# Performance work log

Hardware: AMD Instinct MI355X
Metric: run time of the kernel (lower is better)

Reference implementation:

```python
import jax, jax.numpy as jnp
import numpy as np

B, N = 8, 4096  # batch of epidemic trajectories, nodes in the contact network


def setup_inputs() -> dict:
    key = jax.random.key(0)
    k1, k2, k3, k4 = jax.random.split(key, 4)
    state = jax.random.uniform(k1, (B, 4, N), dtype=jnp.float32)
    state = state / state.sum(axis=1, keepdims=True)  # per-node SEIR distribution
    ISNet = jax.random.uniform(k2, (N, N), dtype=jnp.float32)  # dense contact weights in [0,1)
    # small transition probs so rows sum < 1 (expand_psMatrix stays a valid stochastic matrix)
    psMatrix = jax.random.uniform(k3, (4, 4), dtype=jnp.float32) * 0.05
    U = jax.random.uniform(k4, (N,), dtype=jnp.float32)  # torch.rand(n) draw, shared across batch
    return {"state": state, "ISNet": ISNet, "psMatrix": psMatrix, "U": U}


def _expand_ps(psMatrix):
    # eye * (1 - row_sum) + psMatrix  (adds the stay-in-state probability)
    stable = 1.0 - psMatrix.sum(axis=1)
    return jnp.eye(4, dtype=psMatrix.dtype) * stable + psMatrix


def _step(state, ISNet, psMatrix):
    psM = _expand_ps(psMatrix)
    p01 = psM[0, 1]
    # lp[b,j,k] = log(1 - ISNet[j,k] * S_b[j] * I_b[k] * p01)   (vectorized over batch)
    lp = jnp.log(1.0 - ISNet[None, :, :] * state[:, 0, :, None] * state[:, 2, None, :] * p01)
    ps1 = 1.0 - jnp.exp(lp.sum(axis=2))  # [B, N] infection probability per node
    zeros = jnp.zeros_like(ps1)
    ps10 = jnp.stack([1.0 - ps1, ps1, zeros, zeros], axis=1)  # [B, 4, N]
    # constantM zeroes the S row of psM before the transpose-matmul
    mask = jnp.array([[0.0, 0, 0, 0], [1, 1, 1, 1], [1, 1, 1, 1], [1, 1, 1, 1]], dtype=psM.dtype)
    ps2T = (psM * mask).T  # [4, 4]
    return state[:, 0][:, None, :] * ps10 + jnp.einsum('ij,bjn->bin', ps2T, state)


def _sample(P, U):
    # cumulative-threshold sampling: first compartment whose running sum crosses U fires
    u = jnp.broadcast_to(U[None, :], P[:, 0, :].shape)  # [B, N], shared draw across batch
    outs = []
    for i in range(P.shape[1]):  # fixed 4 compartments
        u = u - P[:, i, :]
        s = (u < 0).astype(P.dtype)
        outs.append(s)
        u = u + s
    return jnp.stack(outs, axis=1)  # [B, 4, N] one-hot per node


def reference(state, ISNet, psMatrix, U):
    new_state = _step(state, ISNet, psMatrix)
    return _sample(new_state, U)
```

## Files before the change

kernel.cpp:

```cpp
#include <hip/hip_runtime.h>

#define NN 4096
#define BB 8
#define JT 4


__device__ __forceinline__ float2 pk_mul(float2 a, float2 b) {
    return make_float2(a.x * b.x, a.y * b.y);
}
__device__ __forceinline__ float2 pk_add(float2 a, float2 b) {
    return make_float2(a.x + b.x, a.y + b.y);
}
__device__ __forceinline__ float2 pk_fnma(float2 a, float2 b, float2 c) {
    return make_float2(fmaf(-a.x, b.x, c.x), fmaf(-a.y, b.y, c.y));
}

__global__ __launch_bounds__(256) void epi_kernel(
    const float* __restrict__ state,
    const float* __restrict__ ISNet,
    const float* __restrict__ psMatrix,
    const float* __restrict__ U,
    float* __restrict__ out)
{
    const int j0   = blockIdx.x * JT;
    const int tid  = threadIdx.x;
    const int wave = tid >> 6;
    const int lane = tid & 63;
    const int b0   = wave * 2;

    const float p01 = psMatrix[1];

    float  cf[JT][2];
    double prod[JT][2];
    #pragma unroll
    for (int jj = 0; jj < JT; ++jj) {
        #pragma unroll
        for (int bi = 0; bi < 2; ++bi) {
            cf[jj][bi]   = state[(size_t)(b0 + bi) * 4 * NN + (j0 + jj)] * p01;
            prod[jj][bi] = 1.0;
        }
    }

    const float4* __restrict__ w0 = (const float4*)(ISNet + (size_t)(j0 + 0) * NN);
    const float4* __restrict__ w1 = (const float4*)(ISNet + (size_t)(j0 + 1) * NN);
    const float4* __restrict__ w2 = (const float4*)(ISNet + (size_t)(j0 + 2) * NN);
    const float4* __restrict__ w3 = (const float4*)(ISNet + (size_t)(j0 + 3) * NN);
    const float4* __restrict__ i0 = (const float4*)(state + ((size_t)(b0 + 0) * 4 + 2) * NN);
    const float4* __restrict__ i1 = (const float4*)(state + ((size_t)(b0 + 1) * 4 + 2) * NN);

    float4 wA[JT], wB[JT], iA[2], iB[2];

#define LOADSET(W, I, X)                                   \
    do {                                                   \
        const int _x = (X);                                \
        W[0] = w0[_x]; W[1] = w1[_x];                      \
        W[2] = w2[_x]; W[3] = w3[_x];                      \
        I[0] = i0[_x]; I[1] = i1[_x];                      \
    } while (0)

    auto compute = [&](const float4 (&W)[JT], const float4 (&I)[2]) {
        #pragma unroll
        for (int jj = 0; jj < JT; ++jj) {
            const float2 w01 = make_float2(W[jj].x, W[jj].y);
            const float2 w23 = make_float2(W[jj].z, W[jj].w);
            #pragma unroll
            for (int bi = 0; bi < 2; ++bi) {
                const float2 c2  = make_float2(cf[jj][bi], cf[jj][bi]);
                const float2 i01 = make_float2(I[bi].x, I[bi].y);
                const float2 i23 = make_float2(I[bi].z, I[bi].w);
                const float2 z01 = pk_mul(pk_mul(c2, w01), i01);
                const float2 z23 = pk_mul(pk_mul(c2, w23), i23);
                const float2 q2 = pk_fnma(z01, z23, pk_add(z01, z23));
                const float q = fmaf(-q2.x, q2.y, q2.x + q2.y);
                prod[jj][bi] = fma(-(double)q, prod[jj][bi], prod[jj][bi]);
            }
        }
    };

    LOADSET(wA, iA, lane);
    LOADSET(wB, iB, lane + 64);
    #pragma unroll
    for (int it = 0; it < 16; it += 2) {
        compute(wA, iA);
        if (it + 2 < 16) LOADSET(wA, iA, lane + (it + 2) * 64);
        compute(wB, iB);
        if (it + 3 < 16) LOADSET(wB, iB, lane + (it + 3) * 64);
    }
#undef LOADSET

    #pragma unroll
    for (int off = 32; off > 0; off >>= 1) {
        #pragma unroll
        for (int jj = 0; jj < JT; ++jj) {
            #pragma unroll
            for (int bi = 0; bi < 2; ++bi)
                prod[jj][bi] *= __shfl_down(prod[jj][bi], off, 64);
        }
    }

    __shared__ double red[JT][BB];
    if (lane == 0) {
        #pragma unroll
        for (int jj = 0; jj < JT; ++jj) {
            #pragma unroll
            for (int bi = 0; bi < 2; ++bi)
                red[jj][b0 + bi] = prod[jj][bi];
        }
    }
    __syncthreads();

    if (tid < JT * BB) {
        const int jj = tid >> 3, b = tid & 7;
        const int j  = j0 + jj;
        const double tot = red[jj][b];
        const double ps1 = 1.0 - tot;

        double pm[4][4];
        #pragma unroll
        for (int r = 0; r < 4; ++r) {
            double s = 0.0;
            #pragma unroll
            for (int q = 0; q < 4; ++q) {
                pm[r][q] = (double)psMatrix[r * 4 + q];
                s += pm[r][q];
            }
            pm[r][r] += (1.0 - s);
        }

        double st[4];
        #pragma unroll
        for (int r = 0; r < 4; ++r)
            st[r] = (double)state[(size_t)b * 4 * NN + r * NN + j];

        const double S = st[0];
        const double ps10[4] = {1.0 - ps1, ps1, 0.0, 0.0};

        double P[4];
        #pragma unroll
        for (int i = 0; i < 4; ++i) {
            double acc = S * ps10[i];
            #pragma unroll
            for (int r = 1; r < 4; ++r)
                acc += pm[r][i] * st[r];
            P[i] = acc;
        }

        double u = (double)U[j];
        #pragma unroll
        for (int i = 0; i < 4; ++i) {
            u -= P[i];
            const double s = (u < 0.0) ? 1.0 : 0.0;
            out[(size_t)b * 4 * NN + i * NN + j] = (float)s;
            u += s;
        }
    }
}

extern "C" void kernel_launch(void* const* d_in, const int* in_sizes, int n_in,
                              void* d_out, int out_size, void* d_ws, size_t ws_size,
                              hipStream_t stream) {
    const float* state    = (const float*)d_in[0];
    const float* ISNet    = (const float*)d_in[1];
    const float* psMatrix = (const float*)d_in[2];
    const float* U        = (const float*)d_in[3];
    float* out            = (float*)d_out;

    epi_kernel<<<NN / JT, 256, 0, stream>>>(state, ISNet, psMatrix, U, out);
}
```

Baseline: 24.18 us.

## Triple-buffer weight loads, split I loads, and use transpose-style wave reduction

Replaces the double-buffered combined loads with three rotating ISNet weight buffers prefetched three steps ahead and two I buffers prefetched two steps ahead. The goal is to hide more global memory latency. The per-wave reduction is reworked: xor shuffles reduce down to 8-lane groups, then each group selects one of the eight (j,b) products and finishes with three shuffles, which cuts total shuffle count. Launch bounds now request 4 blocks per CU, which may limit registers and cause spills given the extra buffers.

Measured after the change: 23.98 us. About the same (-0.9%).

```diff
diff --git a/kernel.cpp b/kernel.cpp
--- a/kernel.cpp
+++ b/kernel.cpp
@@ -15,7 +15,7 @@
     return make_float2(fmaf(-a.x, b.x, c.x), fmaf(-a.y, b.y, c.y));
 }
 
-__global__ __launch_bounds__(256) void epi_kernel(
+__global__ __launch_bounds__(256, 4) void epi_kernel(
     const float* __restrict__ state,
     const float* __restrict__ ISNet,
     const float* __restrict__ psMatrix,
@@ -48,14 +48,18 @@
     const float4* __restrict__ i0 = (const float4*)(state + ((size_t)(b0 + 0) * 4 + 2) * NN);
     const float4* __restrict__ i1 = (const float4*)(state + ((size_t)(b0 + 1) * 4 + 2) * NN);
 
-    float4 wA[JT], wB[JT], iA[2], iB[2];
+    float4 wA[JT], wB[JT], wC[JT], ia[2], ib[2];
 
-#define LOADSET(W, I, X)                                   \
-    do {                                                   \
-        const int _x = (X);                                \
-        W[0] = w0[_x]; W[1] = w1[_x];                      \
-        W[2] = w2[_x]; W[3] = w3[_x];                      \
-        I[0] = i0[_x]; I[1] = i1[_x];                      \
+#define LW(BUF, IDX)                                        \
+    do {                                                    \
+        const int _x = lane + (IDX) * 64;                   \
+        BUF[0] = w0[_x]; BUF[1] = w1[_x];                   \
+        BUF[2] = w2[_x]; BUF[3] = w3[_x];                   \
+    } while (0)
+#define LI(BUF, IDX)                                        \
+    do {                                                    \
+        const int _x = lane + (IDX) * 64;                   \
+        BUF[0] = i0[_x]; BUF[1] = i1[_x];                   \
     } while (0)
 
     auto compute = [&](const float4 (&W)[JT], const float4 (&I)[2]) {
@@ -70,43 +74,56 @@
                 const float2 i23 = make_float2(I[bi].z, I[bi].w);
                 const float2 z01 = pk_mul(pk_mul(c2, w01), i01);
                 const float2 z23 = pk_mul(pk_mul(c2, w23), i23);
-                const float2 q2 = pk_fnma(z01, z23, pk_add(z01, z23));
-                const float q = fmaf(-q2.x, q2.y, q2.x + q2.y);
+                const float2 q2  = pk_fnma(z01, z23, pk_add(z01, z23));
+                const float  q   = fmaf(-q2.x, q2.y, q2.x + q2.y);
                 prod[jj][bi] = fma(-(double)q, prod[jj][bi], prod[jj][bi]);
             }
         }
     };
 
-    LOADSET(wA, iA, lane);
-    LOADSET(wB, iB, lane + 64);
-    #pragma unroll
-    for (int it = 0; it < 16; it += 2) {
-        compute(wA, iA);
-        if (it + 2 < 16) LOADSET(wA, iA, lane + (it + 2) * 64);
-        compute(wB, iB);
-        if (it + 3 < 16) LOADSET(wB, iB, lane + (it + 3) * 64);
-    }
-#undef LOADSET
+#define STEP(W, I, K)                                       \
+    do {                                                    \
+        compute(W, I);                                      \
+        if ((K) + 3 < 16) LW(W, (K) + 3);                   \
+        if ((K) + 2 < 16) LI(I, (K) + 2);                   \
+    } while (0)
+
+    LW(wA, 0); LI(ia, 0); LW(wB, 1); LI(ib, 1); LW(wC, 2);
+
+    STEP(wA, ia, 0);  STEP(wB, ib, 1);  STEP(wC, ia, 2);  STEP(wA, ib, 3);
+    STEP(wB, ia, 4);  STEP(wC, ib, 5);  STEP(wA, ia, 6);  STEP(wB, ib, 7);
+    STEP(wC, ia, 8);  STEP(wA, ib, 9);  STEP(wB, ia, 10); STEP(wC, ib, 11);
+    STEP(wA, ia, 12); STEP(wB, ib, 13); STEP(wC, ia, 14); STEP(wA, ib, 15);
+#undef STEP
+#undef LW
+#undef LI
 
     #pragma unroll
-    for (int off = 32; off > 0; off >>= 1) {
+    for (int off = 32; off >= 8; off >>= 1) {
         #pragma unroll
         for (int jj = 0; jj < JT; ++jj) {
             #pragma unroll
             for (int bi = 0; bi < 2; ++bi)
-                prod[jj][bi] *= __shfl_down(prod[jj][bi], off, 64);
+                prod[jj][bi] *= __shfl_xor(prod[jj][bi], off, 64);
         }
     }
 
+    const int g = lane >> 3;
+    double v = prod[0][0];
+    v = (g == 1) ? prod[0][1] : v;
+    v = (g == 2) ? prod[1][0] : v;
+    v = (g == 3) ? prod[1][1] : v;
+    v = (g == 4) ? prod[2][0] : v;
+    v = (g == 5) ? prod[2][1] : v;
+    v = (g == 6) ? prod[3][0] : v;
+    v = (g == 7) ? prod[3][1] : v;
+    v *= __shfl_down(v, 4, 64);
+    v *= __shfl_down(v, 2, 64);
+    v *= __shfl_down(v, 1, 64);
+
     __shared__ double red[JT][BB];
-    if (lane == 0) {
-        #pragma unroll
-        for (int jj = 0; jj < JT; ++jj) {
-            #pragma unroll
-            for (int bi = 0; bi < 2; ++bi)
-                red[jj][b0 + bi] = prod[jj][bi];
-        }
-    }
+    if ((lane & 7) == 0)
+        red[g >> 1][b0 + (g & 1)] = v;
     __syncthreads();
 
     if (tid < JT * BB) {
```
